# Performance work log

Hardware: AMD Instinct MI355X
Metric: run time of the kernel (lower is better)

## Reference

```python
import jax, jax.numpy as jnp
import numpy as np

EMBED_DIM = 1024
NUM_HEADS = 16
HEAD_DIM = EMBED_DIM // NUM_HEADS
HIDDEN_DIM = 4096


def layer_norm(x, gamma, beta, eps=1e-5):
    mu = jnp.mean(x, axis=-1, keepdims=True)
    var = jnp.var(x, axis=-1, keepdims=True)
    return (x - mu) * jax.lax.rsqrt(var + eps) * gamma + beta


def setup_inputs() -> dict:
    key = jax.random.key(0)
    ks = jax.random.split(key, 12)
    D, H3, F = EMBED_DIM, 3 * EMBED_DIM, HIDDEN_DIM
    s_d = 1.0 / np.sqrt(D)
    s_f = 1.0 / np.sqrt(F)
    return {
        "x": jax.random.normal(ks[0], (2, 2048, D), dtype=jnp.float32),
        "w_qkv": jax.random.uniform(ks[1], (D, H3), jnp.float32, -s_d, s_d),
        "b_qkv": jax.random.uniform(ks[2], (H3,), jnp.float32, -s_d, s_d),
        "w_out": jax.random.uniform(ks[3], (D, D), jnp.float32, -s_d, s_d),
        "b_out": jax.random.uniform(ks[4], (D,), jnp.float32, -s_d, s_d),
        "w_fc1": jax.random.uniform(ks[5], (D, F), jnp.float32, -s_d, s_d),
        "b_fc1": jax.random.uniform(ks[6], (F,), jnp.float32, -s_d, s_d),
        "w_fc2": jax.random.uniform(ks[7], (F, D), jnp.float32, -s_f, s_f),
        "b_fc2": jax.random.uniform(ks[8], (D,), jnp.float32, -s_f, s_f),
        "ln1_g": jnp.ones((D,), jnp.float32),
        "ln1_b": jnp.zeros((D,), jnp.float32),
        "ln2_g": jnp.ones((D,), jnp.float32),
        "ln2_b": jnp.zeros((D,), jnp.float32),
    }


def reference(x, w_qkv, b_qkv, w_out, b_out, w_fc1, b_fc1, w_fc2, b_fc2,
              ln1_g, ln1_b, ln2_g, ln2_b):
    B, N, D = x.shape
    H, Hd = NUM_HEADS, HEAD_DIM

    # --- attention branch (pre-LN) ---
    h = layer_norm(x, ln1_g, ln1_b)
    qkv = h @ w_qkv + b_qkv                              # [B,N,3D]
    qkv = qkv.reshape(B, N, 3, H, Hd).transpose(2, 0, 3, 1, 4)  # [3,B,H,N,Hd]
    q, k, v = qkv[0], qkv[1], qkv[2]
    scores = jnp.einsum("bhnd,bhmd->bhnm", q, k) * (Hd ** -0.5)  # [B,H,N,N]
    attn = jax.nn.softmax(scores, axis=-1)
    out = jnp.einsum("bhnm,bhmd->bhnd", attn, v)         # [B,H,N,Hd]
    out = out.transpose(0, 2, 1, 3).reshape(B, N, D)
    x = x + (out @ w_out + b_out)

    # --- FFN branch (pre-LN) ---
    h = layer_norm(x, ln2_g, ln2_b)
    h = jax.nn.gelu(h @ w_fc1 + b_fc1, approximate=False)  # torch F.gelu default (erf)
    x = x + (h @ w_fc2 + b_fc2)
    return x
```

## Files before the change

### kernel.cpp

```cpp
#include <hip/hip_runtime.h>
#include <hip/hip_bf16.h>

#define D_ 1024
#define F_ 4096
#define NH 16
#define HD 64
#define SEQ 2048
#define TOK 4096

typedef short bf16x8 __attribute__((ext_vector_type(8)));
typedef float f32x4 __attribute__((ext_vector_type(4)));
typedef unsigned int u32x4 __attribute__((ext_vector_type(4)));

static __device__ __forceinline__ f32x4 mfma16(bf16x8 a, bf16x8 b, f32x4 c) {
  return __builtin_amdgcn_mfma_f32_16x16x32_bf16(a, b, c, 0, 0, 0);
}

static __device__ __forceinline__ unsigned short f2bf(float f) {
  union { float f; unsigned int u; } a; a.f = f;
  unsigned int u = a.u;
  u += 0x7fffu + ((u >> 16) & 1u);
  return (unsigned short)(u >> 16);
}

static __device__ __forceinline__ unsigned int cvtpk(float lo, float hi) {
  unsigned int r;
  asm("v_cvt_pk_bf16_f32 %0, %1, %2" : "=v"(r) : "v"(lo), "v"(hi));
  return r;
}

#define AS1 __attribute__((address_space(1)))
#define AS3 __attribute__((address_space(3)))
static __device__ __forceinline__ void gld16(const void* g, void* l) {
  __builtin_amdgcn_global_load_lds((const AS1 unsigned int*)(uintptr_t)(g),
                                   (AS3 unsigned int*)(uintptr_t)(l), 16, 0, 0);
}

#define WAITBAR_CNT()                                    \
  do {                                                   \
    asm volatile("s_waitcnt vmcnt(4)" ::: "memory");     \
    __builtin_amdgcn_s_barrier();                        \
    __builtin_amdgcn_sched_barrier(0);                   \
  } while (0)
#define WAITBAR0()                                       \
  do {                                                   \
    asm volatile("s_waitcnt vmcnt(0)" ::: "memory");     \
    __builtin_amdgcn_s_barrier();                        \
    __builtin_amdgcn_sched_barrier(0);                   \
  } while (0)

__global__ void transpose_all(const float* __restrict__ wqkv, const float* __restrict__ wout,
                              const float* __restrict__ wfc1, const float* __restrict__ wfc2,
                              unsigned short* __restrict__ oqkv, unsigned short* __restrict__ oout,
                              unsigned short* __restrict__ ofc1, unsigned short* __restrict__ ofc2) {
  __shared__ float tile[32][33];
  int idx = blockIdx.x;
  const float* in;
  unsigned short* out;
  int K, N;
  if (idx < 3072)      { in = wqkv; out = oqkv; K = 1024; N = 3072; }
  else if (idx < 4096) { in = wout; out = oout; K = 1024; N = 1024; idx -= 3072; }
  else if (idx < 8192) { in = wfc1; out = ofc1; K = 1024; N = 4096; idx -= 4096; }
  else                 { in = wfc2; out = ofc2; K = 4096; N = 1024; idx -= 8192; }
  int nt = N >> 5;
  int n0 = (idx % nt) * 32, k0 = (idx / nt) * 32;
  int tx = threadIdx.x, ty = threadIdx.y;
#pragma unroll
  for (int i = 0; i < 32; i += 8)
    tile[ty + i][tx] = in[(size_t)(k0 + ty + i) * N + n0 + tx];
  __syncthreads();
#pragma unroll
  for (int i = 0; i < 32; i += 8)
    out[(size_t)(n0 + ty + i) * K + k0 + tx] = f2bf(tile[tx][ty + i]);
}

__global__ __launch_bounds__(256) void layernorm_bf16(const float* __restrict__ x,
                                                      const float* __restrict__ g,
                                                      const float* __restrict__ bta,
                                                      unsigned short* __restrict__ out) {
  int wv = threadIdx.x >> 6, lane = threadIdx.x & 63;
  int row = blockIdx.x * 4 + wv;
  const float4* xr = (const float4*)(x + (size_t)row * D_);
  float4 v[4];
  float s = 0.f, ss = 0.f;
#pragma unroll
  for (int i = 0; i < 4; i++) {
    v[i] = xr[i * 64 + lane];
    s += v[i].x + v[i].y + v[i].z + v[i].w;
    ss += v[i].x * v[i].x + v[i].y * v[i].y + v[i].z * v[i].z + v[i].w * v[i].w;
  }
#pragma unroll
  for (int off = 32; off >= 1; off >>= 1) {
    s += __shfl_xor(s, off);
    ss += __shfl_xor(ss, off);
  }
  float mu = s * (1.0f / D_);
  float var = ss * (1.0f / D_) - mu * mu;
  float r = rsqrtf(var + 1e-5f);
#pragma unroll
  for (int i = 0; i < 4; i++) {
    int col = i * 256 + lane * 4;
    unsigned short ob[4];
    ob[0] = f2bf((v[i].x - mu) * r * g[col + 0] + bta[col + 0]);
    ob[1] = f2bf((v[i].y - mu) * r * g[col + 1] + bta[col + 1]);
    ob[2] = f2bf((v[i].z - mu) * r * g[col + 2] + bta[col + 2]);
    ob[3] = f2bf((v[i].w - mu) * r * g[col + 3] + bta[col + 3]);
    *(ushort4*)(out + (size_t)row * D_ + col) = *(ushort4*)ob;
  }
}

__global__ __launch_bounds__(256) void ln2_fused(const float* __restrict__ xin,
                                                 const float* __restrict__ p,
                                                 const float* __restrict__ g,
                                                 const float* __restrict__ bta,
                                                 float* __restrict__ x1out,
                                                 unsigned short* __restrict__ out) {
  int wv = threadIdx.x >> 6, lane = threadIdx.x & 63;
  int row = blockIdx.x * 4 + wv;
  const float4* xr = (const float4*)(xin + (size_t)row * D_);
  const float4* pr = (const float4*)(p + (size_t)row * D_);
  float4* xw = (float4*)(x1out + (size_t)row * D_);
  float4 v[4];
  float s = 0.f, ss = 0.f;
#pragma unroll
  for (int i = 0; i < 4; i++) {
    float4 a = xr[i * 64 + lane], b = pr[i * 64 + lane];
    v[i] = make_float4(a.x + b.x, a.y + b.y, a.z + b.z, a.w + b.w);
    xw[i * 64 + lane] = v[i];
    s += v[i].x + v[i].y + v[i].z + v[i].w;
    ss += v[i].x * v[i].x + v[i].y * v[i].y + v[i].z * v[i].z + v[i].w * v[i].w;
  }
#pragma unroll
  for (int off = 32; off >= 1; off >>= 1) {
    s += __shfl_xor(s, off);
    ss += __shfl_xor(ss, off);
  }
  float mu = s * (1.0f / D_);
  float var = ss * (1.0f / D_) - mu * mu;
  float r = rsqrtf(var + 1e-5f);
#pragma unroll
  for (int i = 0; i < 4; i++) {
    int col = i * 256 + lane * 4;
    unsigned short ob[4];
    ob[0] = f2bf((v[i].x - mu) * r * g[col + 0] + bta[col + 0]);
    ob[1] = f2bf((v[i].y - mu) * r * g[col + 1] + bta[col + 1]);
    ob[2] = f2bf((v[i].z - mu) * r * g[col + 2] + bta[col + 2]);
    ob[3] = f2bf((v[i].w - mu) * r * g[col + 3] + bta[col + 3]);
    *(ushort4*)(out + (size_t)row * D_ + col) = *(ushort4*)ob;
  }
}

__global__ __launch_bounds__(256) void reduce_add(float4* __restrict__ out,
                                                  const float4* __restrict__ p1) {
#pragma unroll
  for (int j = 0; j < 4; ++j) {
    int i = blockIdx.x * 1024 + j * 256 + threadIdx.x;
    float4 o = out[i], a = p1[i];
    out[i] = make_float4(o.x + a.x, o.y + a.y, o.z + a.z, o.w + a.w);
  }
}

template <int MODE, int NBUF>
__global__ __launch_bounds__(256, (NBUF == 2 ? 4 : 3)) void gemm_bt(
    const unsigned short* __restrict__ A, const unsigned short* __restrict__ Bt,
    const float* __restrict__ bias, const float* __restrict__ resid,
    void* __restrict__ outp, float* __restrict__ p1, int M, int N, int K, int KSPL) {
  __shared__ __align__(16) char lds_all[NBUF * 16384];
  char* const a_lds = lds_all;
  char* const b_lds = lds_all + NBUF * 8192;
  const int t = threadIdx.x;
  const int lane = t & 63, w = t >> 6;
  const int g = lane >> 4, lr = lane & 15;
  const int wm = (w >> 1) * 64, wn = (w & 1) * 64;
  const int n0 = blockIdx.x * 128, m0 = blockIdx.y * 128;
  const int z = blockIdx.z;
  const int kt0 = z * KSPL, nIter = KSPL / 32;

  const int mac0 = t >> 3;
  const int v0 = ((t & 7) ^ (mac0 & 7)) << 4;
  const int grow0 = mac0 + ((v0 >> 6) << 6);
  const int cc0 = v0 & 63;
  const char* srcA0 = (const char*)A + ((size_t)(m0 + grow0) * K + kt0) * 2 + cc0;
  const char* srcA1 = srcA0 + (size_t)32 * K * 2;
  const char* srcB0 = (const char*)Bt + ((size_t)(n0 + grow0) * K + kt0) * 2 + cc0;
  const char* srcB1 = srcB0 + (size_t)32 * K * 2;

  const int rdA = lr * 128 + (((wm & 64) + g * 16) ^ ((lr & 7) << 4));
  const int rdB = lr * 128 + (((wn & 64) + g * 16) ^ ((lr & 7) << 4));

#define STAGE(IT, BO)                                                    \
  do {                                                                   \
    size_t kb = (size_t)(IT) * 64;                                       \
    gld16(srcA0 + kb, a_lds + (BO) + t * 16);                            \
    gld16(srcA1 + kb, a_lds + (BO) + 4096 + t * 16);                     \
    gld16(srcB0 + kb, b_lds + (BO) + t * 16);                            \
    gld16(srcB1 + kb, b_lds + (BO) + 4096 + t * 16);                     \
  } while (0)

#define GSTEP(BO)                                                          \
  do {                                                                     \
    bf16x8 af[4], bfr[4];                                                  \
    _Pragma("unroll") for (int mi = 0; mi < 4; mi++)                       \
        af[mi] = *(const bf16x8*)(a_lds + (BO) + rdA + mi * 2048);         \
    _Pragma("unroll") for (int ni = 0; ni < 4; ni++)                       \
        bfr[ni] = *(const bf16x8*)(b_lds + (BO) + rdB + ni * 2048);        \
    _Pragma("unroll") for (int mi = 0; mi < 4; mi++)                       \
        _Pragma("unroll") for (int ni = 0; ni < 4; ni++)                   \
            acc[mi][ni] = mfma16(af[mi], bfr[ni], acc[mi][ni]);            \
  } while (0)

  f32x4 acc[4][4] = {};
  if constexpr (NBUF == 2) {
    STAGE(0, 0);
    int cur = 0;
#pragma unroll 1
    for (int it = 0; it < nIter; ++it) {
      WAITBAR0();
      if (it + 1 < nIter) STAGE(it + 1, (cur ^ 1) * 8192);
      GSTEP(cur * 8192);
      cur ^= 1;
    }
  } else {
    STAGE(0, 0);
    STAGE(1, 8192);
    int bo0 = 0, bo1 = 8192, bo2 = 16384;
#pragma unroll 1
    for (int it = 0; it < nIter - 1; ++it) {
      WAITBAR_CNT();
      if (it + 2 < nIter) STAGE(it + 2, bo2);
      GSTEP(bo0);
      int tmp = bo0; bo0 = bo1; bo1 = bo2; bo2 = tmp;
    }
    WAITBAR0();
    GSTEP(bo0);
  }
#undef STAGE
#undef GSTEP

  if (MODE == 0) {
    const int whichB = n0 >> 10;
    if (whichB == 2) {
      __syncthreads();
#pragma unroll
      for (int mi = 0; mi < 4; mi++) {
        int colbase = wm + mi * 16 + g * 4;
        int off = colbase & 63;
        int cpos = (off & 35) | ((off & 4) << 1) | ((off & 8) << 1) | ((off & 16) >> 2);
        int nplb = ((colbase & 64) + cpos) * 2;
#pragma unroll
        for (int ni = 0; ni < 4; ni++) {
          int rl = wn + ni * 16 + lr;
          float bia = bias[n0 + rl];
          unsigned short v4[4];
#pragma unroll
          for (int j = 0; j < 4; j++) v4[j] = f2bf(acc[mi][ni][j] + bia);
          int byt = rl * 256 + (nplb ^ ((rl & 7) << 4));
          *(unsigned long long*)(lds_all + byt) = *(const unsigned long long*)v4;
        }
      }
      __syncthreads();
      int r = t >> 1, half = t & 1;
      int hh = ((n0 & 1023) >> 6) + (r >> 6);
      int dd = r & 63;
      int bb = m0 >> 11;
      char* dst = (char*)outp +
                  2 * ((size_t)2 * TOK * D_ +
                       ((size_t)(bb * NH + hh) * HD + dd) * SEQ + (m0 & 2047) + half * 64);
#pragma unroll
      for (int c = 0; c < 8; c++) {
        int src = r * 256 + ((half * 128 + c * 16) ^ ((r & 7) << 4));
        *(int4*)(dst + c * 16) = *(const int4*)(lds_all + src);
      }
    } else {
#pragma unroll
      for (int mi = 0; mi < 4; mi++) {
#pragma unroll
        for (int ni = 0; ni < 4; ni++) {
#pragma unroll
          for (int j = 0; j < 4; j++) {
            int row = m0 + wm + mi * 16 + g * 4 + j;
            int col = n0 + wn + ni * 16 + lr;
            float val = acc[mi][ni][j] + bias[col];
            int cc = col & 1023;
            int hh = cc >> 6, dd = cc & 63;
            int bb = row >> 11, nn = row & 2047;
            if (whichB == 0) val *= 0.18033688011112042f;
            ((unsigned short*)outp)[(size_t)whichB * (TOK * D_) +
                                    (((size_t)(bb * NH + hh) * SEQ + nn) << 6) + dd] =
                f2bf(val);
          }
        }
      }
    }
    return;
  }

#pragma unroll
  for (int mi = 0; mi < 4; mi++) {
#pragma unroll
    for (int ni = 0; ni < 4; ni++) {
#pragma unroll
      for (int j = 0; j < 4; j++) {
        int row = m0 + wm + mi * 16 + g * 4 + j;
        int col = n0 + wn + ni * 16 + lr;
        float val = acc[mi][ni][j];
        if (MODE == 2) {
          val += bias[col];
          val = 0.5f * val * (1.0f + erff(val * 0.70710678118f));
          ((unsigned short*)outp)[(size_t)row * N + col] = f2bf(val);
        } else if (MODE == 5 || MODE == 6) {
          if (z == 0) {
            val += bias[col] + resid[(size_t)row * N + col];
            ((float*)outp)[(size_t)row * N + col] = val;
          } else {
            p1[(size_t)row * N + col] = val;
          }
        }
      }
    }
  }
}

__global__ __launch_bounds__(256, 4) void attn_kernel(const unsigned short* __restrict__ q,
                                                      const unsigned short* __restrict__ k,
                                                      const unsigned short* __restrict__ vT,
                                                      unsigned short* __restrict__ ao) {
  __shared__ __align__(16) char ldsb[32768];
  const int t = threadIdx.x, lane = t & 63, w = t >> 6;
  const int g = lane >> 4, lr = lane & 15;
  const int bid = (blockIdx.x & 7) * 128 + (blockIdx.x >> 3);
  const int qt = bid & 31, bh = bid >> 5;
  const int bb = bh >> 4, hh = bh & 15;

  const unsigned short* qp = q + ((size_t)bh * SEQ + qt * 64 + w * 16) * HD;
  bf16x8 qf0 = *(const bf16x8*)(qp + lr * HD + g * 8);
  bf16x8 qf1 = *(const bf16x8*)(qp + lr * HD + 32 + g * 8);

  f32x4 oacc[4] = {};
  f32x4 spv = {0.f, 0.f, 0.f, 0.f};

  const int srow = t >> 3, sc = (t & 7) << 4;
  const int ssw = sc ^ ((srow & 7) << 4);
  const char* kgl = (const char*)(k + (size_t)bh * SEQ * HD) + srow * 128 + ssw;
  const char* vgl = (const char*)(vT + (size_t)bh * HD * SEQ) + (size_t)srow * 4096 + ssw;
  char* kdst = ldsb + w * 1024;
  char* vdst = ldsb + 16384 + w * 1024;

  const int rsw = (lr & 7) << 4;
  const char* r0 = ldsb + lr * 128 + ((g * 16) ^ rsw);
  const char* r1 = ldsb + lr * 128 + ((64 + g * 16) ^ rsw);

#define ISSUE(BUF)                                   \
  do {                                               \
    gld16(kgl, kdst + (BUF) * 8192);                 \
    gld16(kgl + 4096, kdst + (BUF) * 8192 + 4096);   \
    gld16(vgl, vdst + (BUF) * 8192);                 \
    gld16(vgl + 131072, vdst + (BUF) * 8192 + 4096); \
    kgl += 8192;                                     \
    vgl += 128;                                      \
  } while (0)

#define COMPUTE(BUF)                                                                     \
  do {                                                                                   \
    f32x4 sT[4];                                                                         \
    __builtin_amdgcn_s_setprio(1);                                                       \
    _Pragma("unroll") for (int sb = 0; sb < 4; ++sb) {                                   \
      bf16x8 kf0 = *(const bf16x8*)(r0 + (BUF) * 8192 + sb * 2048);                      \
      bf16x8 kf1 = *(const bf16x8*)(r1 + (BUF) * 8192 + sb * 2048);                      \
      f32x4 zz = {};                                                                     \
      zz = mfma16(kf0, qf0, zz);                                                         \
      sT[sb] = mfma16(kf1, qf1, zz);                                                     \
    }                                                                                    \
    __builtin_amdgcn_s_setprio(0);                                                       \
    float p[4][4];                                                                       \
    _Pragma("unroll") for (int sb = 0; sb < 4; ++sb) _Pragma("unroll")                   \
        for (int jr = 0; jr < 4; ++jr) {                                                 \
      p[sb][jr] = exp2f(sT[sb][jr]);                                                     \
      spv[jr] += p[sb][jr];                                                              \
    }                                                                                    \
    u32x4 pA[2];                                                                         \
    _Pragma("unroll") for (int kk = 0; kk < 2; ++kk) pA[kk] =                            \
        (u32x4){cvtpk(p[2 * kk][0], p[2 * kk][1]), cvtpk(p[2 * kk][2], p[2 * kk][3]),    \
                cvtpk(p[2 * kk + 1][0], p[2 * kk + 1][1]),                               \
                cvtpk(p[2 * kk + 1][2], p[2 * kk + 1][3])};                              \
    __builtin_amdgcn_s_setprio(1);                                                       \
    _Pragma("unroll") for (int vb = 0; vb < 4; ++vb) {                                   \
      bf16x8 v0 = *(const bf16x8*)(r0 + 16384 + (BUF) * 8192 + vb * 2048);               \
      bf16x8 v1 = *(const bf16x8*)(r1 + 16384 + (BUF) * 8192 + vb * 2048);               \
      oacc[vb] = mfma16(__builtin_bit_cast(bf16x8, pA[0]), v0, oacc[vb]);                \
      oacc[vb] = mfma16(__builtin_bit_cast(bf16x8, pA[1]), v1, oacc[vb]);                \
    }                                                                                    \
    __builtin_amdgcn_s_setprio(0);                                                       \
  } while (0)

  ISSUE(0);

  int staged = 1;
#pragma unroll 1
  for (int i2 = 0; i2 < SEQ / 128; ++i2) {
    WAITBAR0();
    if (staged < SEQ / 64) { ISSUE(1); ++staged; }
    COMPUTE(0);
    WAITBAR0();
    if (staged < SEQ / 64) { ISSUE(0); ++staged; }
    COMPUTE(1);
  }
#undef ISSUE
#undef COMPUTE

  float sp = (spv[0] + spv[1]) + (spv[2] + spv[3]);
  sp += __shfl_xor(sp, 16);
  sp += __shfl_xor(sp, 32);

#pragma unroll
  for (int jj = 0; jj < 4; ++jj) {
    float li = 1.0f / __shfl(sp, g * 4 + jj);
    int nrow = qt * 64 + w * 16 + g * 4 + jj;
#pragma unroll
    for (int vb = 0; vb < 4; ++vb)
      ao[((size_t)bb * SEQ + nrow) * D_ + hh * HD + vb * 16 + lr] = f2bf(oacc[vb][jj] * li);
  }
}

extern "C" void kernel_launch(void* const* d_in, const int* in_sizes, int n_in,
                              void* d_out, int out_size, void* d_ws, size_t ws_size,
                              hipStream_t stream) {
  const float* x     = (const float*)d_in[0];
  const float* w_qkv = (const float*)d_in[1];
  const float* b_qkv = (const float*)d_in[2];
  const float* w_out = (const float*)d_in[3];
  const float* b_out = (const float*)d_in[4];
  const float* w_fc1 = (const float*)d_in[5];
  const float* b_fc1 = (const float*)d_in[6];
  const float* w_fc2 = (const float*)d_in[7];
  const float* b_fc2 = (const float*)d_in[8];
  const float* ln1_g = (const float*)d_in[9];
  const float* ln1_b = (const float*)d_in[10];
  const float* ln2_g = (const float*)d_in[11];
  const float* ln2_b = (const float*)d_in[12];
  float* out = (float*)d_out;

  char* ws = (char*)d_ws;
  unsigned short* wqkvT = (unsigned short*)(ws);
  unsigned short* woutT = (unsigned short*)(ws + 6291456);
  unsigned short* wfc1T = (unsigned short*)(ws + 8388608);
  unsigned short* wfc2T = (unsigned short*)(ws + 16777216);
  unsigned short* h     = (unsigned short*)(ws + 25165824);
  unsigned short* qkv   = (unsigned short*)(ws + 33554432);
  unsigned short* ao    = (unsigned short*)(ws + 58720256);
  float*          x1    = (float*)(ws + 67108864);
  unsigned short* hg    = (unsigned short*)(ws + 83886080);
  float* p_op  = (float*)(ws + 83886080);
  float* p_fc1 = (float*)(ws);

  transpose_all<<<12288, dim3(32, 8), 0, stream>>>(w_qkv, w_out, w_fc1, w_fc2,
                                                   wqkvT, woutT, wfc1T, wfc2T);

  layernorm_bf16<<<TOK / 4, 256, 0, stream>>>(x, ln1_g, ln1_b, h);
  gemm_bt<0, 3><<<dim3(24, 32, 1), 256, 0, stream>>>(h, wqkvT, b_qkv, nullptr, qkv, nullptr,
                                                     TOK, 3072, 1024, 1024);
  attn_kernel<<<1024, 256, 0, stream>>>(qkv, qkv + (size_t)TOK * D_, qkv + 2 * (size_t)TOK * D_,
                                        ao);
  gemm_bt<5, 3><<<dim3(8, 32, 2), 256, 0, stream>>>(ao, woutT, b_out, x, x1, p_op,
                                                    TOK, 1024, 1024, 512);
  ln2_fused<<<TOK / 4, 256, 0, stream>>>(x1, p_op, ln2_g, ln2_b, x1, h);
  gemm_bt<2, 2><<<dim3(32, 32, 1), 256, 0, stream>>>(h, wfc1T, b_fc1, nullptr, hg, nullptr,
                                                     TOK, 4096, 1024, 1024);
  gemm_bt<6, 3><<<dim3(8, 32, 2), 256, 0, stream>>>(hg, wfc2T, b_fc2, x1, out, p_fc1,
                                                    TOK, 1024, 4096, 2048);
  reduce_add<<<1024, 256, 0, stream>>>((float4*)out, (const float4*)p_fc1);
}
```

Baseline: 261.0 us.

## Replace split-K with 128x64 tiles for N=1024 GEMMs, drop reduction kernels

The two N=1024 GEMMs (attention out-projection and FC2) no longer use two-way split-K with partial buffers. They use a narrower 128x64 output tile, giving 512 blocks instead of 256x2, and fuse bias plus residual directly in the epilogue. This removes the ln2_fused add pass and the final reduce_add kernel, and the second layernorm now reuses the plain layernorm kernel on x1. In exchange each block runs the full K loop, which is long for FC2 (K=4096), and the narrower tile does fewer MFMAs per LDS load.

```diff
diff --git a/kernel.cpp b/kernel.cpp
--- a/kernel.cpp
+++ b/kernel.cpp
@@ -36,12 +36,6 @@
                                    (AS3 unsigned int*)(uintptr_t)(l), 16, 0, 0);
 }
 
-#define WAITBAR_CNT()                                    \
-  do {                                                   \
-    asm volatile("s_waitcnt vmcnt(4)" ::: "memory");     \
-    __builtin_amdgcn_s_barrier();                        \
-    __builtin_amdgcn_sched_barrier(0);                   \
-  } while (0)
 #define WAITBAR0()                                       \
   do {                                                   \
     asm volatile("s_waitcnt vmcnt(0)" ::: "memory");     \
@@ -109,133 +103,97 @@
   }
 }
 
-__global__ __launch_bounds__(256) void ln2_fused(const float* __restrict__ xin,
-                                                 const float* __restrict__ p,
-                                                 const float* __restrict__ g,
-                                                 const float* __restrict__ bta,
-                                                 float* __restrict__ x1out,
-                                                 unsigned short* __restrict__ out) {
-  int wv = threadIdx.x >> 6, lane = threadIdx.x & 63;
-  int row = blockIdx.x * 4 + wv;
-  const float4* xr = (const float4*)(xin + (size_t)row * D_);
-  const float4* pr = (const float4*)(p + (size_t)row * D_);
-  float4* xw = (float4*)(x1out + (size_t)row * D_);
-  float4 v[4];
-  float s = 0.f, ss = 0.f;
-#pragma unroll
-  for (int i = 0; i < 4; i++) {
-    float4 a = xr[i * 64 + lane], b = pr[i * 64 + lane];
-    v[i] = make_float4(a.x + b.x, a.y + b.y, a.z + b.z, a.w + b.w);
-    xw[i * 64 + lane] = v[i];
-    s += v[i].x + v[i].y + v[i].z + v[i].w;
-    ss += v[i].x * v[i].x + v[i].y * v[i].y + v[i].z * v[i].z + v[i].w * v[i].w;
-  }
-#pragma unroll
-  for (int off = 32; off >= 1; off >>= 1) {
-    s += __shfl_xor(s, off);
-    ss += __shfl_xor(ss, off);
-  }
-  float mu = s * (1.0f / D_);
-  float var = ss * (1.0f / D_) - mu * mu;
-  float r = rsqrtf(var + 1e-5f);
-#pragma unroll
-  for (int i = 0; i < 4; i++) {
-    int col = i * 256 + lane * 4;
-    unsigned short ob[4];
-    ob[0] = f2bf((v[i].x - mu) * r * g[col + 0] + bta[col + 0]);
-    ob[1] = f2bf((v[i].y - mu) * r * g[col + 1] + bta[col + 1]);
-    ob[2] = f2bf((v[i].z - mu) * r * g[col + 2] + bta[col + 2]);
-    ob[3] = f2bf((v[i].w - mu) * r * g[col + 3] + bta[col + 3]);
-    *(ushort4*)(out + (size_t)row * D_ + col) = *(ushort4*)ob;
-  }
-}
-
-__global__ __launch_bounds__(256) void reduce_add(float4* __restrict__ out,
-                                                  const float4* __restrict__ p1) {
-#pragma unroll
-  for (int j = 0; j < 4; ++j) {
-    int i = blockIdx.x * 1024 + j * 256 + threadIdx.x;
-    float4 o = out[i], a = p1[i];
-    out[i] = make_float4(o.x + a.x, o.y + a.y, o.z + a.z, o.w + a.w);
-  }
-}
-
-template <int MODE, int NBUF>
+template <int MODE, int NBUF, int TN>
 __global__ __launch_bounds__(256, (NBUF == 2 ? 4 : 3)) void gemm_bt(
     const unsigned short* __restrict__ A, const unsigned short* __restrict__ Bt,
     const float* __restrict__ bias, const float* __restrict__ resid,
-    void* __restrict__ outp, float* __restrict__ p1, int M, int N, int K, int KSPL) {
-  __shared__ __align__(16) char lds_all[NBUF * 16384];
+    void* __restrict__ outp, int M, int N, int K) {
+  constexpr int BSZ = TN * 64;
+  constexpr int NI = TN / 32;
+  __shared__ __align__(16) char lds_all[NBUF * (8192 + BSZ)];
   char* const a_lds = lds_all;
   char* const b_lds = lds_all + NBUF * 8192;
   const int t = threadIdx.x;
   const int lane = t & 63, w = t >> 6;
   const int g = lane >> 4, lr = lane & 15;
-  const int wm = (w >> 1) * 64, wn = (w & 1) * 64;
-  const int n0 = blockIdx.x * 128, m0 = blockIdx.y * 128;
-  const int z = blockIdx.z;
-  const int kt0 = z * KSPL, nIter = KSPL / 32;
+  const int wm = (w >> 1) * 64, wn = (w & 1) * (TN / 2);
+  const int n0 = blockIdx.x * TN, m0 = blockIdx.y * 128;
+  const int nIter = K / 32;
 
   const int mac0 = t >> 3;
   const int v0 = ((t & 7) ^ (mac0 & 7)) << 4;
-  const int grow0 = mac0 + ((v0 >> 6) << 6);
   const int cc0 = v0 & 63;
-  const char* srcA0 = (const char*)A + ((size_t)(m0 + grow0) * K + kt0) * 2 + cc0;
+  const int growA = mac0 + ((v0 >> 6) << 6);
+  const int growB = mac0 + ((v0 >> 6) << (TN == 128 ? 6 : 5));
+  const char* srcA0 = (const char*)A + ((size_t)(m0 + growA) * K) * 2 + cc0;
   const char* srcA1 = srcA0 + (size_t)32 * K * 2;
-  const char* srcB0 = (const char*)Bt + ((size_t)(n0 + grow0) * K + kt0) * 2 + cc0;
+  const char* srcB0 = (const char*)Bt + ((size_t)(n0 + growB) * K) * 2 + cc0;
   const char* srcB1 = srcB0 + (size_t)32 * K * 2;
 
-  const int rdA = lr * 128 + (((wm & 64) + g * 16) ^ ((lr & 7) << 4));
-  const int rdB = lr * 128 + (((wn & 64) + g * 16) ^ ((lr & 7) << 4));
-
-#define STAGE(IT, BO)                                                    \
-  do {                                                                   \
-    size_t kb = (size_t)(IT) * 64;                                       \
-    gld16(srcA0 + kb, a_lds + (BO) + t * 16);                            \
-    gld16(srcA1 + kb, a_lds + (BO) + 4096 + t * 16);                     \
-    gld16(srcB0 + kb, b_lds + (BO) + t * 16);                            \
-    gld16(srcB1 + kb, b_lds + (BO) + 4096 + t * 16);                     \
-  } while (0)
-
-#define GSTEP(BO)                                                          \
-  do {                                                                     \
-    bf16x8 af[4], bfr[4];                                                  \
-    _Pragma("unroll") for (int mi = 0; mi < 4; mi++)                       \
-        af[mi] = *(const bf16x8*)(a_lds + (BO) + rdA + mi * 2048);         \
-    _Pragma("unroll") for (int ni = 0; ni < 4; ni++)                       \
-        bfr[ni] = *(const bf16x8*)(b_lds + (BO) + rdB + ni * 2048);        \
-    _Pragma("unroll") for (int mi = 0; mi < 4; mi++)                       \
-        _Pragma("unroll") for (int ni = 0; ni < 4; ni++)                   \
-            acc[mi][ni] = mfma16(af[mi], bfr[ni], acc[mi][ni]);            \
-  } while (0)
-
-  f32x4 acc[4][4] = {};
+  const int rsw = (lr & 7) << 4;
+  const int rdA = lr * 128 + (((wm & 64) + g * 16) ^ rsw);
+  const int rdB = lr * 128 + ((((TN == 128) ? (wn & 64) : ((wn & 32) * 2)) + g * 16) ^ rsw);
+
+#define STAGE(IT, BUF)                                                    \
+  do {                                                                    \
+    size_t kb = (size_t)(IT) * 64;                                        \
+    gld16(srcA0 + kb, a_lds + (BUF) * 8192 + t * 16);                     \
+    gld16(srcA1 + kb, a_lds + (BUF) * 8192 + 4096 + t * 16);              \
+    gld16(srcB0 + kb, b_lds + (BUF) * BSZ + t * 16);                      \
+    if constexpr (TN == 128)                                              \
+      gld16(srcB1 + kb, b_lds + (BUF) * BSZ + 4096 + t * 16);             \
+  } while (0)
+
+#define GSTEP(BUF)                                                           \
+  do {                                                                       \
+    bf16x8 af[4], bfr[NI];                                                   \
+    _Pragma("unroll") for (int mi = 0; mi < 4; mi++)                         \
+        af[mi] = *(const bf16x8*)(a_lds + (BUF) * 8192 + rdA + mi * 2048);   \
+    _Pragma("unroll") for (int ni = 0; ni < NI; ni++)                        \
+        bfr[ni] = *(const bf16x8*)(b_lds + (BUF) * BSZ + rdB + ni * 2048);   \
+    _Pragma("unroll") for (int mi = 0; mi < 4; mi++)                         \
+        _Pragma("unroll") for (int ni = 0; ni < NI; ni++)                    \
+            acc[mi][ni] = mfma16(af[mi], bfr[ni], acc[mi][ni]);              \
+  } while (0)
+
+#define WAITBAR_OLD()                                                     \
+  do {                                                                    \
+    if constexpr (TN == 128)                                              \
+      asm volatile("s_waitcnt vmcnt(4)" ::: "memory");                    \
+    else                                                                  \
+      asm volatile("s_waitcnt vmcnt(3)" ::: "memory");                    \
+    __builtin_amdgcn_s_barrier();                                         \
+    __builtin_amdgcn_sched_barrier(0);                                    \
+  } while (0)
+
+  f32x4 acc[4][NI] = {};
   if constexpr (NBUF == 2) {
     STAGE(0, 0);
     int cur = 0;
 #pragma unroll 1
     for (int it = 0; it < nIter; ++it) {
       WAITBAR0();
-      if (it + 1 < nIter) STAGE(it + 1, (cur ^ 1) * 8192);
-      GSTEP(cur * 8192);
+      if (it + 1 < nIter) STAGE(it + 1, cur ^ 1);
+      GSTEP(cur);
       cur ^= 1;
     }
   } else {
     STAGE(0, 0);
-    STAGE(1, 8192);
-    int bo0 = 0, bo1 = 8192, bo2 = 16384;
+    STAGE(1, 1);
+    int b0 = 0, b1 = 1, b2 = 2;
 #pragma unroll 1
     for (int it = 0; it < nIter - 1; ++it) {
-      WAITBAR_CNT();
-      if (it + 2 < nIter) STAGE(it + 2, bo2);
-      GSTEP(bo0);
-      int tmp = bo0; bo0 = bo1; bo1 = bo2; bo2 = tmp;
+      WAITBAR_OLD();
+      if (it + 2 < nIter) STAGE(it + 2, b2);
+      GSTEP(b0);
+      int tmp = b0; b0 = b1; b1 = b2; b2 = tmp;
     }
     WAITBAR0();
-    GSTEP(bo0);
+    GSTEP(b0);
   }
 #undef STAGE
 #undef GSTEP
+#undef WAITBAR_OLD
 
   if (MODE == 0) {
     const int whichB = n0 >> 10;
@@ -248,7 +206,7 @@
         int cpos = (off & 35) | ((off & 4) << 1) | ((off & 8) << 1) | ((off & 16) >> 2);
         int nplb = ((colbase & 64) + cpos) * 2;
 #pragma unroll
-        for (int ni = 0; ni < 4; ni++) {
+        for (int ni = 0; ni < NI; ni++) {
           int rl = wn + ni * 16 + lr;
           float bia = bias[n0 + rl];
           unsigned short v4[4];
@@ -275,7 +233,7 @@
 #pragma unroll
       for (int mi = 0; mi < 4; mi++) {
 #pragma unroll
-        for (int ni = 0; ni < 4; ni++) {
+        for (int ni = 0; ni < NI; ni++) {
 #pragma unroll
           for (int j = 0; j < 4; j++) {
             int row = m0 + wm + mi * 16 + g * 4 + j;
@@ -298,7 +256,7 @@
 #pragma unroll
   for (int mi = 0; mi < 4; mi++) {
 #pragma unroll
-    for (int ni = 0; ni < 4; ni++) {
+    for (int ni = 0; ni < NI; ni++) {
 #pragma unroll
       for (int j = 0; j < 4; j++) {
         int row = m0 + wm + mi * 16 + g * 4 + j;
@@ -308,13 +266,9 @@
           val += bias[col];
           val = 0.5f * val * (1.0f + erff(val * 0.70710678118f));
           ((unsigned short*)outp)[(size_t)row * N + col] = f2bf(val);
-        } else if (MODE == 5 || MODE == 6) {
-          if (z == 0) {
-            val += bias[col] + resid[(size_t)row * N + col];
-            ((float*)outp)[(size_t)row * N + col] = val;
-          } else {
-            p1[(size_t)row * N + col] = val;
-          }
+        } else if (MODE == 5) {
+          val += bias[col] + resid[(size_t)row * N + col];
+          ((float*)outp)[(size_t)row * N + col] = val;
         }
       }
     }
@@ -450,23 +404,20 @@
   unsigned short* ao    = (unsigned short*)(ws + 58720256);
   float*          x1    = (float*)(ws + 67108864);
   unsigned short* hg    = (unsigned short*)(ws + 83886080);
-  float* p_op  = (float*)(ws + 83886080);
-  float* p_fc1 = (float*)(ws);
 
   transpose_all<<<12288, dim3(32, 8), 0, stream>>>(w_qkv, w_out, w_fc1, w_fc2,
                                                    wqkvT, woutT, wfc1T, wfc2T);
 
   layernorm_bf16<<<TOK / 4, 256, 0, stream>>>(x, ln1_g, ln1_b, h);
-  gemm_bt<0, 3><<<dim3(24, 32, 1), 256, 0, stream>>>(h, wqkvT, b_qkv, nullptr, qkv, nullptr,
-                                                     TOK, 3072, 1024, 1024);
+  gemm_bt<0, 3, 128><<<dim3(24, 32), 256, 0, stream>>>(h, wqkvT, b_qkv, nullptr, qkv,
+                                                       TOK, 3072, 1024);
   attn_kernel<<<1024, 256, 0, stream>>>(qkv, qkv + (size_t)TOK * D_, qkv + 2 * (size_t)TOK * D_,
                                         ao);
-  gemm_bt<5, 3><<<dim3(8, 32, 2), 256, 0, stream>>>(ao, woutT, b_out, x, x1, p_op,
-                                                    TOK, 1024, 1024, 512);
-  ln2_fused<<<TOK / 4, 256, 0, stream>>>(x1, p_op, ln2_g, ln2_b, x1, h);
-  gemm_bt<2, 2><<<dim3(32, 32, 1), 256, 0, stream>>>(h, wfc1T, b_fc1, nullptr, hg, nullptr,
-                                                     TOK, 4096, 1024, 1024);
-  gemm_bt<6, 3><<<dim3(8, 32, 2), 256, 0, stream>>>(hg, wfc2T, b_fc2, x1, out, p_fc1,
-                                                    TOK, 1024, 4096, 2048);
-  reduce_add<<<1024, 256, 0, stream>>>((float4*)out, (const float4*)p_fc1);
-}
+  gemm_bt<5, 3, 64><<<dim3(16, 32), 256, 0, stream>>>(ao, woutT, b_out, x, x1,
+                                                      TOK, 1024, 1024);
+  layernorm_bf16<<<TOK / 4, 256, 0, stream>>>(x1, ln2_g, ln2_b, h);
+  gemm_bt<2, 2, 128><<<dim3(32, 32), 256, 0, stream>>>(h, wfc1T, b_fc1, nullptr, hg,
+                                                       TOK, 4096, 1024);
+  gemm_bt<5, 3, 64><<<dim3(16, 32), 256, 0, stream>>>(hg, wfc2T, b_fc2, x1, out,
+                                                      TOK, 1024, 4096);
+}
```

New measurement: 244.1 us. -6.5%, faster.
